# Optimization experiments

Hardware: AMD Instinct MI355X
Metric: run time of the kernel (lower is better)

## Reference

```python
import jax, jax.numpy as jnp
import numpy as np

B, P, S, H, R = 32, 512, 1024, 1024, 256


def setup_inputs() -> dict:
    key = jax.random.key(0)
    k1, k2, k3 = jax.random.split(key, 3)
    pairs = jax.random.randint(k1, (B, P, 2, 2), 0, S, dtype=jnp.int64 if jax.config.jax_enable_x64 else jnp.int32)
    hidden_states = jax.random.normal(k2, (B, S, H), dtype=jnp.float32)
    W = jax.random.normal(k3, (R, 3 * H), dtype=jnp.float32) * (1.0 / np.sqrt(3 * H))
    b = jnp.zeros((R,), dtype=jnp.float32)
    return {"pairs": pairs, "hidden_states": hidden_states, "W": W, "b": b}


def reference(pairs, hidden_states, W, b):
    # pairs: [B, P, 2, 2] -> [:, :, 0, :] = (h_start, h_end), [:, :, 1, :] = (t_start, t_end)
    def gather_tokens(idx):  # idx: [B, P] -> [B, P, H]
        return jnp.take_along_axis(hidden_states, idx[:, :, None], axis=1)

    head_embed = 0.5 * (gather_tokens(pairs[:, :, 0, 0]) + gather_tokens(pairs[:, :, 0, 1]))
    tail_embed = 0.5 * (gather_tokens(pairs[:, :, 1, 0]) + gather_tokens(pairs[:, :, 1, 1]))
    feats = jnp.concatenate([head_embed, tail_embed, head_embed * tail_embed], axis=-1)  # [B, P, 3H]
    logits = jnp.einsum('bpf,rf->bpr', feats, W) + b  # [B, P, R]
    return logits
```

## Files before the change

kernel.cpp:

```cpp
#include <hip/hip_runtime.h>

#define NB 32
#define NP 512
#define NS 1024
#define NH 1024
#define NR 256
#define K3 3072

#define BM 64
#define BK 64
#define KP 72

typedef short short8 __attribute__((ext_vector_type(8)));
typedef __bf16 bf16x8 __attribute__((ext_vector_type(8)));
typedef float f32x4 __attribute__((ext_vector_type(4)));

__device__ __forceinline__ unsigned short f2bf(float f) {
  unsigned u = __builtin_bit_cast(unsigned, f);
  u += 0x7fffu + ((u >> 16) & 1u);
  return (unsigned short)(u >> 16);
}

__device__ __forceinline__ f32x4 mfma_bf16(short8 a, short8 b, f32x4 c) {
  return __builtin_amdgcn_mfma_f32_16x16x32_bf16(
      __builtin_bit_cast(bf16x8, a), __builtin_bit_cast(bf16x8, b), c, 0, 0, 0);
}

__global__ void wconv_kernel(const float* __restrict__ W,
                             unsigned short* __restrict__ WbF) {
  int i = blockIdx.x * blockDim.x + threadIdx.x;
  int lane = i & 63, n16 = (i >> 6) & 15, kc = i >> 10;
  int lr = lane & 15, lg = lane >> 4;
  const float* src = W + (size_t)(n16 * 16 + lr) * K3 + kc * 32 + lg * 8;
  float4 a = *(const float4*)src;
  float4 b = *(const float4*)(src + 4);
  short8 o;
  o[0] = (short)f2bf(a.x); o[1] = (short)f2bf(a.y);
  o[2] = (short)f2bf(a.z); o[3] = (short)f2bf(a.w);
  o[4] = (short)f2bf(b.x); o[5] = (short)f2bf(b.y);
  o[6] = (short)f2bf(b.z); o[7] = (short)f2bf(b.w);
  *(short8*)(WbF + (size_t)i * 8) = o;
}

__global__ __launch_bounds__(512, 2) void gemm_kernel(
    const int* __restrict__ pairs, const float* __restrict__ hs,
    const unsigned short* __restrict__ WbF, const float* __restrict__ bias,
    float* __restrict__ out) {
  __shared__ __align__(16) unsigned short sA[2][3][BM][KP];
  __shared__ int sPair[BM][4];

  const int tid   = threadIdx.x;
  const int blk   = blockIdx.x;
  const int batch = blk >> 3;
  const int m0    = blk * BM;

  if (tid < BM) {
    int4 pr = ((const int4*)pairs)[m0 + tid];
    sPair[tid][0] = pr.x; sPair[tid][1] = pr.y;
    sPair[tid][2] = pr.z; sPair[tid][3] = pr.w;
  }
  __syncthreads();

  const int arow = tid >> 3;
  const int q    = tid & 7;
  const float* hb  = hs + (size_t)batch * NS * NH;
  const float* pr0 = hb + (size_t)sPair[arow][0] * NH + q * 8;
  const float* pr1 = hb + (size_t)sPair[arow][1] * NH + q * 8;
  const float* pr2 = hb + (size_t)sPair[arow][2] * NH + q * 8;
  const float* pr3 = hb + (size_t)sPair[arow][3] * NH + q * 8;

  const int lane = tid & 63;
  const int w    = tid >> 6;
  const int lr   = lane & 15;
  const int lg   = lane >> 4;

  const unsigned short* wb = WbF + (size_t)(w * 2) * 512 + (size_t)lane * 8;

  f32x4 acc[4][2];
#pragma unroll
  for (int i = 0; i < 4; ++i)
#pragma unroll
    for (int j = 0; j < 2; ++j) acc[i][j] = (f32x4){0.f, 0.f, 0.f, 0.f};

  float4 ld[8];

  auto load_tiles = [&](int k0) {
    ld[0] = *(const float4*)(pr0 + k0);  ld[1] = *(const float4*)(pr0 + k0 + 4);
    ld[2] = *(const float4*)(pr1 + k0);  ld[3] = *(const float4*)(pr1 + k0 + 4);
    ld[4] = *(const float4*)(pr2 + k0);  ld[5] = *(const float4*)(pr2 + k0 + 4);
    ld[6] = *(const float4*)(pr3 + k0);  ld[7] = *(const float4*)(pr3 + k0 + 4);
  };

  auto store_tiles = [&](int buf) {
    short8 hv, tv, pv;
#pragma unroll
    for (int c = 0; c < 8; ++c) {
      const int v = c >> 2, e = c & 3;
      float x0 = ((const float*)&ld[v])[e];
      float x1 = ((const float*)&ld[2 + v])[e];
      float y0 = ((const float*)&ld[4 + v])[e];
      float y1 = ((const float*)&ld[6 + v])[e];
      float h = 0.5f * (x0 + x1);
      float t = 0.5f * (y0 + y1);
      float p = h * t;
      hv[c] = (short)f2bf(h); tv[c] = (short)f2bf(t); pv[c] = (short)f2bf(p);
    }
    const int c0 = q * 8;
    *(short8*)&sA[buf][0][arow][c0] = hv;
    *(short8*)&sA[buf][1][arow][c0] = tv;
    *(short8*)&sA[buf][2][arow][c0] = pv;
  };

  load_tiles(0);
  store_tiles(0);

  for (int kt = 0; kt < 16; ++kt) {
    __syncthreads();
    const int buf = kt & 1;
    if (kt < 15) load_tiles(kt * BK + BK);

#pragma unroll
    for (int ks = 0; ks < 2; ++ks) {
      const int koff = ks * 32 + lg * 8;
      short8 ah[4], at4[4], ap[4];
#pragma unroll
      for (int i = 0; i < 4; ++i) {
        ah[i]  = *(const short8*)&sA[buf][0][i * 16 + lr][koff];
        at4[i] = *(const short8*)&sA[buf][1][i * 16 + lr][koff];
        ap[i]  = *(const short8*)&sA[buf][2][i * 16 + lr][koff];
      }
#pragma unroll
      for (int j = 0; j < 2; ++j) {
        const unsigned short* wp = wb + (size_t)(kt * 2 + ks) * 8192 + (size_t)j * 512;
        short8 b0 = *(const short8*)(wp);
        short8 b1 = *(const short8*)(wp + 32 * 8192);
        short8 b2 = *(const short8*)(wp + 64 * 8192);
#pragma unroll
        for (int i = 0; i < 4; ++i) {
          acc[i][j] = mfma_bf16(ah[i],  b0, acc[i][j]);
          acc[i][j] = mfma_bf16(at4[i], b1, acc[i][j]);
          acc[i][j] = mfma_bf16(ap[i],  b2, acc[i][j]);
        }
      }
    }
    if (kt < 15) store_tiles(buf ^ 1);
  }

#pragma unroll
  for (int j = 0; j < 2; ++j) {
    const int col  = w * 32 + j * 16 + lr;
    const float bv = bias[col];
#pragma unroll
    for (int i = 0; i < 4; ++i) {
      const size_t rbase = (size_t)(m0 + i * 16 + lg * 4) * NR + col;
#pragma unroll
      for (int r = 0; r < 4; ++r)
        out[rbase + (size_t)r * NR] = acc[i][j][r] + bv;
    }
  }
}

extern "C" void kernel_launch(void* const* d_in, const int* in_sizes, int n_in,
                              void* d_out, int out_size, void* d_ws, size_t ws_size,
                              hipStream_t stream) {
  const int*   pairs = (const int*)d_in[0];
  const float* hs    = (const float*)d_in[1];
  const float* W     = (const float*)d_in[2];
  const float* bias  = (const float*)d_in[3];
  float* out = (float*)d_out;
  unsigned short* WbF = (unsigned short*)d_ws;

  wconv_kernel<<<(96 * 16 * 64) / 256, 256, 0, stream>>>(W, WbF);
  gemm_kernel<<<(NB * NP) / BM, 512, 0, stream>>>(pairs, hs, WbF, bias, out);
}
```

Baseline: 247.3 us.

## Swizzle block-to-batch mapping, load pair indices per thread, interleave gather columns

Remaps block indices so that consecutive blocks on different XCDs handle different batches, grouping each batch's tiles together to improve L2 locality for the hidden-state gathers. Each thread now reads its pair indices directly from global memory, which removes the shared-memory staging and one barrier. The gather assigns each thread two 4-float chunks 32 columns apart rather than 8 contiguous floats, so a row's loads are spread across the threads of a quad, and the LDS stores become 8-byte writes. Bank conflicts on the LDS writes and coalescing patterns may change.

```diff
diff --git a/kernel.cpp b/kernel.cpp
--- a/kernel.cpp
+++ b/kernel.cpp
@@ -12,6 +12,7 @@
 #define KP 72
 
 typedef short short8 __attribute__((ext_vector_type(8)));
+typedef short short4v __attribute__((ext_vector_type(4)));
 typedef __bf16 bf16x8 __attribute__((ext_vector_type(8)));
 typedef float f32x4 __attribute__((ext_vector_type(4)));
 
@@ -47,27 +48,24 @@
     const unsigned short* __restrict__ WbF, const float* __restrict__ bias,
     float* __restrict__ out) {
   __shared__ __align__(16) unsigned short sA[2][3][BM][KP];
-  __shared__ int sPair[BM][4];
 
-  const int tid   = threadIdx.x;
-  const int blk   = blockIdx.x;
-  const int batch = blk >> 3;
-  const int m0    = blk * BM;
+  const int tid = threadIdx.x;
+  const int blk = blockIdx.x;
+  const int x     = blk & 7;
+  const int jb    = blk >> 3;
+  const int batch = x * 4 + (jb >> 3);
+  const int mtile = jb & 7;
+  const int m0    = (batch * 8 + mtile) * BM;
 
-  if (tid < BM) {
-    int4 pr = ((const int4*)pairs)[m0 + tid];
-    sPair[tid][0] = pr.x; sPair[tid][1] = pr.y;
-    sPair[tid][2] = pr.z; sPair[tid][3] = pr.w;
-  }
-  __syncthreads();
-
-  const int arow = tid >> 3;
-  const int q    = tid & 7;
-  const float* hb  = hs + (size_t)batch * NS * NH;
-  const float* pr0 = hb + (size_t)sPair[arow][0] * NH + q * 8;
-  const float* pr1 = hb + (size_t)sPair[arow][1] * NH + q * 8;
-  const float* pr2 = hb + (size_t)sPair[arow][2] * NH + q * 8;
-  const float* pr3 = hb + (size_t)sPair[arow][3] * NH + q * 8;
+  const int pairi = tid >> 3;
+  const int q     = tid & 7;
+  int4 pr = ((const int4*)pairs)[m0 + pairi];
+  const float* hb = hs + (size_t)batch * NS * NH;
+  const float* rp[4];
+  rp[0] = hb + (size_t)pr.x * NH + 4 * q;
+  rp[1] = hb + (size_t)pr.y * NH + 4 * q;
+  rp[2] = hb + (size_t)pr.z * NH + 4 * q;
+  rp[3] = hb + (size_t)pr.w * NH + 4 * q;
 
   const int lane = tid & 63;
   const int w    = tid >> 6;
@@ -84,40 +82,38 @@
 
   float4 ld[8];
 
-  auto load_tiles = [&](int k0) {
-    ld[0] = *(const float4*)(pr0 + k0);  ld[1] = *(const float4*)(pr0 + k0 + 4);
-    ld[2] = *(const float4*)(pr1 + k0);  ld[3] = *(const float4*)(pr1 + k0 + 4);
-    ld[4] = *(const float4*)(pr2 + k0);  ld[5] = *(const float4*)(pr2 + k0 + 4);
-    ld[6] = *(const float4*)(pr3 + k0);  ld[7] = *(const float4*)(pr3 + k0 + 4);
+  auto load_stage = [&](int s) {
+    const int o = s * BK;
+#pragma unroll
+    for (int jj = 0; jj < 8; ++jj)
+      ld[jj] = *(const float4*)(rp[jj >> 1] + o + 32 * (jj & 1));
   };
 
-  auto store_tiles = [&](int buf) {
-    short8 hv, tv, pv;
+  auto store_stage = [&](int buf) {
 #pragma unroll
-    for (int c = 0; c < 8; ++c) {
-      const int v = c >> 2, e = c & 3;
-      float x0 = ((const float*)&ld[v])[e];
-      float x1 = ((const float*)&ld[2 + v])[e];
-      float y0 = ((const float*)&ld[4 + v])[e];
-      float y1 = ((const float*)&ld[6 + v])[e];
-      float h = 0.5f * (x0 + x1);
-      float t = 0.5f * (y0 + y1);
-      float p = h * t;
-      hv[c] = (short)f2bf(h); tv[c] = (short)f2bf(t); pv[c] = (short)f2bf(p);
+    for (int c = 0; c < 2; ++c) {
+      short4v hv, tv, pv;
+#pragma unroll
+      for (int e = 0; e < 4; ++e) {
+        float h = 0.5f * (((const float*)&ld[0 + c])[e] + ((const float*)&ld[2 + c])[e]);
+        float t = 0.5f * (((const float*)&ld[4 + c])[e] + ((const float*)&ld[6 + c])[e]);
+        float p = h * t;
+        hv[e] = (short)f2bf(h); tv[e] = (short)f2bf(t); pv[e] = (short)f2bf(p);
+      }
+      const int c0 = 4 * q + 32 * c;
+      *(short4v*)&sA[buf][0][pairi][c0] = hv;
+      *(short4v*)&sA[buf][1][pairi][c0] = tv;
+      *(short4v*)&sA[buf][2][pairi][c0] = pv;
     }
-    const int c0 = q * 8;
-    *(short8*)&sA[buf][0][arow][c0] = hv;
-    *(short8*)&sA[buf][1][arow][c0] = tv;
-    *(short8*)&sA[buf][2][arow][c0] = pv;
   };
 
-  load_tiles(0);
-  store_tiles(0);
+  load_stage(0);
+  store_stage(0);
 
-  for (int kt = 0; kt < 16; ++kt) {
+  for (int s = 0; s < 16; ++s) {
     __syncthreads();
-    const int buf = kt & 1;
-    if (kt < 15) load_tiles(kt * BK + BK);
+    const int buf = s & 1;
+    if (s < 15) load_stage(s + 1);
 
 #pragma unroll
     for (int ks = 0; ks < 2; ++ks) {
@@ -131,7 +127,7 @@
       }
 #pragma unroll
       for (int j = 0; j < 2; ++j) {
-        const unsigned short* wp = wb + (size_t)(kt * 2 + ks) * 8192 + (size_t)j * 512;
+        const unsigned short* wp = wb + (size_t)(s * 2 + ks) * 8192 + (size_t)j * 512;
         short8 b0 = *(const short8*)(wp);
         short8 b1 = *(const short8*)(wp + 32 * 8192);
         short8 b2 = *(const short8*)(wp + 64 * 8192);
@@ -143,7 +139,7 @@
         }
       }
     }
-    if (kt < 15) store_tiles(buf ^ 1);
+    if (s < 15) store_stage(buf ^ 1);
   }
 
 #pragma unroll
```

New measurement: 239.4 us. -3.2%, faster.
